# Performance work log

Measured on AMD Instinct MI355X. Metric: run time of the kernel, lower is better.

The kernel has to match this reference:

```python
import jax, jax.numpy as jnp
import numpy as np


def setup_inputs() -> dict:
    key = jax.random.key(0)
    attn = jax.random.uniform(key, (64, 1024, 1024), dtype=jnp.float32)
    return {"attn": attn}


def reference(attn) -> jnp.ndarray:
    # attn: [B, N, N]. For each sample, group strictly-upper-triangular
    # elements by diagonal offset k = j - i (k = 1..N-2; the k = N-1
    # diagonal has a single element and is excluded, matching the torch
    # loop `for i in range(len(distance_record) - 1)`).
    # For offset k: std (unbiased, ddof=1) of diag elements scaled by
    # (N-k)/5, i.e. std(x) * (N-k)/5. Then mean over k, then mean over B.
    B, N = attn.shape[0], attn.shape[1]
    ii = jnp.arange(N)
    off = ii[None, :] - ii[:, None]              # [N, N], j - i
    upper = off >= 1                              # strict upper triangle
    seg = jnp.where(upper, off, 0).reshape(-1)    # segment id per element
    m = upper.reshape(-1).astype(attn.dtype)      # mask lower/diag to 0

    x = attn.reshape(B, -1) * m                   # [B, N*N]
    segsum = lambda v: jax.ops.segment_sum(v, seg, num_segments=N)
    s1 = jax.vmap(segsum)(x)                      # [B, N] per-offset sums
    s2 = jax.vmap(segsum)(x * x)                  # [B, N] per-offset sum sq

    n = (N - jnp.arange(N)).astype(attn.dtype)    # count per offset k
    mean = s1 / n
    denom = jnp.maximum(n - 1.0, 1.0)             # ddof=1; guard k=N-1 (excluded)
    var = jnp.maximum(s2 - n * mean * mean, 0.0) / denom
    std = jnp.sqrt(var) * (n / 5.0)               # std of scaled values

    per_sample = jnp.mean(std[:, 1:N - 1], axis=1)  # offsets 1..N-2
    return jnp.mean(per_sample)
```

## Files before the change

kernel.cpp:

```cpp
#include <hip/hip_runtime.h>


#define NN 1024
#define NB 64
#define W 1032

__global__ __launch_bounds__(256) void diag_pass1(
    const float* __restrict__ attn, float* __restrict__ ws) {
  const int b  = blockIdx.x >> 3;
  const int c0 = blockIdx.x & 7;
  const int t  = threadIdx.x;
  int p = (4 - (c0 & 3)) & 3; if (p == 0) p = 4;

  const float* __restrict__ base = attn + ((size_t)b << 20);
  const size_t stride = (size_t)16 * (NN + 1);

  const int qB = 255 - t;
  float a1x=0.f,a1y=0.f,a1z=0.f,a1w=0.f,a2x=0.f,a2y=0.f,a2z=0.f,a2w=0.f;
  float b1x=0.f,b1y=0.f,b1z=0.f,b1w=0.f,b2x=0.f,b2y=0.f,b2z=0.f,b2w=0.f;

  #pragma unroll
  for (int h = 0; h < 2; ++h) {
    const int c = c0 + 8 * h;
    const float* __restrict__ rowc = base + (size_t)c * (NN + 1);

    const int dfA = 1020 - c - p - 4 * t;
    const int TfA = (dfA >= 0) ? ((dfA >> 4) + 1) : 0;
    const int SaA = (TfA + 1) >> 1;
    {
      const float* ptr = rowc + (p + 4 * t);
      #pragma unroll 8
      for (int m = 0; m < SaA; ++m) {
        const float4 v = *reinterpret_cast<const float4*>(ptr + (size_t)m * stride);
        a1x += v.x; a2x += v.x * v.x;
        a1y += v.y; a2y += v.y * v.y;
        a1z += v.z; a2z += v.z * v.z;
        a1w += v.w; a2w += v.w * v.w;
      }
    }

    const int dfB = 4 * t - c - p;
    const int TfB = (dfB >= 0) ? ((dfB >> 4) + 1) : 0;
    const int SaB = (TfB + 1) >> 1;
    {
      const float* ptr = rowc + (p + 4 * qB);
      #pragma unroll 8
      for (int m = SaB; m < TfB; ++m) {
        const float4 v = *reinterpret_cast<const float4*>(ptr + (size_t)m * stride);
        b1x += v.x; b2x += v.x * v.x;
        b1y += v.y; b2y += v.y * v.y;
        b1z += v.z; b2z += v.z * v.z;
        b1w += v.w; b2w += v.w * v.w;
      }
    }
  }

  __shared__ float4 lb1[256], lb2[256];
  lb1[qB] = make_float4(b1x, b1y, b1z, b1w);
  lb2[qB] = make_float4(b2x, b2y, b2z, b2w);
  __syncthreads();
  const float4 f1 = lb1[t];
  const float4 f2 = lb2[t];
  a1x += f1.x; a1y += f1.y; a1z += f1.z; a1w += f1.w;
  a2x += f2.x; a2y += f2.y; a2z += f2.z; a2w += f2.w;

  float* __restrict__ w1 = ws + (size_t)blockIdx.x * (2 * W);
  *reinterpret_cast<float4*>(w1 + 4 * t)     = make_float4(a1x,a1y,a1z,a1w);
  *reinterpret_cast<float4*>(w1 + W + 4 * t) = make_float4(a2x,a2y,a2z,a2w);

  const int e = t >> 6;
  if (e >= 1 && e < p) {
    const int l = t & 63;
    float e1 = 0.f, e2 = 0.f;
    #pragma unroll
    for (int h = 0; h < 2; ++h) {
      const int i = c0 + 8 * h + 16 * l;
      if (i + e < NN) {
        const float x = base[(size_t)i * (NN + 1) + e];
        e1 += x; e2 += x * x;
      }
    }
    #pragma unroll
    for (int s = 1; s < 64; s <<= 1) {
      e1 += __shfl_xor(e1, s);
      e2 += __shfl_xor(e2, s);
    }
    if (l == 0) {
      w1[1024 + e]     = e1;
      w1[W + 1024 + e] = e2;
    }
  }
}

__global__ __launch_bounds__(256) void diag_pass2(
    const float* __restrict__ ws, float* __restrict__ part) {
  const int b  = blockIdx.x >> 4;
  const int kg = blockIdx.x & 15;
  const int t  = threadIdx.x;
  const int kk = t & 63;
  const int cg = t >> 6;
  const int k  = kg * 64 + kk;

  int p = (4 - cg) & 3; if (p == 0) p = 4;
  const int idx = (k >= p) ? (k - p) : (1024 + k);

  float s1 = 0.f, s2 = 0.f;
  #pragma unroll
  for (int c = cg; c < 8; c += 4) {
    const float* __restrict__ w0 = ws + (size_t)(b * 8 + c) * (2 * W);
    s1 += w0[idx];
    s2 += w0[W + idx];
  }

  __shared__ float r1[256], r2[256];
  r1[t] = s1; r2[t] = s2;
  __syncthreads();
  if (t < 128) { r1[t] += r1[t + 128]; r2[t] += r2[t + 128]; }
  __syncthreads();
  if (t < 64) {
    s1 = r1[t] + r1[t + 64];
    s2 = r2[t] + r2[t + 64];
    float acc = 0.f;
    if (k >= 1 && k <= NN - 2) {
      const float n = (float)(NN - k);
      const float mean = s1 / n;
      const float var = fmaxf(s2 - n * mean * mean, 0.f) / (n - 1.f);
      acc = sqrtf(var) * (n * 0.2f);
    }
    #pragma unroll
    for (int s = 32; s > 0; s >>= 1) acc += __shfl_down(acc, s);
    if (t == 0) part[blockIdx.x] = acc;
  }
}

__global__ __launch_bounds__(256) void diag_pass3(
    const float* __restrict__ part, float* __restrict__ out) {
  const int t = threadIdx.x;
  float v = part[t] + part[t + 256] + part[t + 512] + part[t + 768];
  __shared__ float red[256];
  red[t] = v;
  __syncthreads();
  #pragma unroll
  for (int s = 128; s > 0; s >>= 1) {
    if (t < s) red[t] += red[t + s];
    __syncthreads();
  }
  if (t == 0) out[0] = red[0] * (1.0f / (1022.0f * 64.0f));
}

extern "C" void kernel_launch(void* const* d_in, const int* in_sizes, int n_in,
                              void* d_out, int out_size, void* d_ws, size_t ws_size,
                              hipStream_t stream) {
  const float* attn = (const float*)d_in[0];
  float* out = (float*)d_out;
  float* ws = (float*)d_ws;

  float* part = ws + (size_t)NB * 8 * 2 * W;

  diag_pass1<<<NB * 8, 256, 0, stream>>>(attn, ws);
  diag_pass2<<<NB * 16, 256, 0, stream>>>(ws, part);
  diag_pass3<<<1, 256, 0, stream>>>(part, out);
}
```

Baseline: 36.68 us.

## Rework diagonal pass to contiguous row bands with per-thread phase accumulators

Pass 1 now gives each block two contiguous 64-row bands, one from the top and one from the bottom of the matrix, which balances the triangular work. It replaces the strided diagonal walk across 16 rows. Each thread reads along rows with four alignment phases and keeps 7 partial sums, which are combined in shared memory into per-offset sums with an explicit fix-up for small offsets. This aims to improve memory locality and load balance, and it simplifies indexing in pass 2. The cost is more shared memory, extra reduction logic and branchy bounds checks per row.

```diff
diff --git a/kernel.cpp b/kernel.cpp
--- a/kernel.cpp
+++ b/kernel.cpp
@@ -3,91 +3,100 @@
 
 #define NN 1024
 #define NB 64
-#define W 1032
+#define WP 1032
 
 __global__ __launch_bounds__(256) void diag_pass1(
     const float* __restrict__ attn, float* __restrict__ ws) {
-  const int b  = blockIdx.x >> 3;
-  const int c0 = blockIdx.x & 7;
-  const int t  = threadIdx.x;
-  int p = (4 - (c0 & 3)) & 3; if (p == 0) p = 4;
+  const int b = blockIdx.x >> 3;
+  const int u = blockIdx.x & 7;
+  const int t = threadIdx.x;
+  const float* __restrict__ base = attn + ((size_t)b << 20);
 
-  const float* __restrict__ base = attn + ((size_t)b << 20);
-  const size_t stride = (size_t)16 * (NN + 1);
+  const int topi = 64 * u;
+  const int boti = 960 - 64 * u;
 
-  const int qB = 255 - t;
-  float a1x=0.f,a1y=0.f,a1z=0.f,a1w=0.f,a2x=0.f,a2y=0.f,a2z=0.f,a2w=0.f;
-  float b1x=0.f,b1y=0.f,b1z=0.f,b1w=0.f,b2x=0.f,b2y=0.f,b2z=0.f,b2w=0.f;
+  float s1[7] = {0.f,0.f,0.f,0.f,0.f,0.f,0.f};
+  float s2[7] = {0.f,0.f,0.f,0.f,0.f,0.f,0.f};
 
+#define ROW1(i, P)                                                        \
+  {                                                                       \
+    const int lim = 1024 - (i) - (P);                                     \
+    if (4 * t < lim) {                                                    \
+      const float4 v = *reinterpret_cast<const float4*>(                  \
+          base + (size_t)(i) * 1025 + (P) + 4 * t);                       \
+      s1[(P) - 1] += v.x; s2[(P) - 1] += v.x * v.x;                       \
+      s1[(P)    ] += v.y; s2[(P)    ] += v.y * v.y;                       \
+      s1[(P) + 1] += v.z; s2[(P) + 1] += v.z * v.z;                       \
+      s1[(P) + 2] += v.w; s2[(P) + 2] += v.w * v.w;                       \
+    }                                                                     \
+  }
+#define ROW4(i0)                                                          \
+  { ROW1((i0), 4) ROW1((i0) + 1, 3) ROW1((i0) + 2, 2) ROW1((i0) + 3, 1) }
+
+  #pragma unroll 2
+  for (int g = 0; g < 16; ++g) {
+    ROW4(topi + 4 * g)
+    ROW4(boti + 4 * g)
+  }
+#undef ROW4
+#undef ROW1
+
+  __shared__ float L1[7 * 256], L2[7 * 256];
+  __shared__ float Eb[8];
   #pragma unroll
-  for (int h = 0; h < 2; ++h) {
-    const int c = c0 + 8 * h;
-    const float* __restrict__ rowc = base + (size_t)c * (NN + 1);
-
-    const int dfA = 1020 - c - p - 4 * t;
-    const int TfA = (dfA >= 0) ? ((dfA >> 4) + 1) : 0;
-    const int SaA = (TfA + 1) >> 1;
-    {
-      const float* ptr = rowc + (p + 4 * t);
-      #pragma unroll 8
-      for (int m = 0; m < SaA; ++m) {
-        const float4 v = *reinterpret_cast<const float4*>(ptr + (size_t)m * stride);
-        a1x += v.x; a2x += v.x * v.x;
-        a1y += v.y; a2y += v.y * v.y;
-        a1z += v.z; a2z += v.z * v.z;
-        a1w += v.w; a2w += v.w * v.w;
-      }
-    }
-
-    const int dfB = 4 * t - c - p;
-    const int TfB = (dfB >= 0) ? ((dfB >> 4) + 1) : 0;
-    const int SaB = (TfB + 1) >> 1;
-    {
-      const float* ptr = rowc + (p + 4 * qB);
-      #pragma unroll 8
-      for (int m = SaB; m < TfB; ++m) {
-        const float4 v = *reinterpret_cast<const float4*>(ptr + (size_t)m * stride);
-        b1x += v.x; b2x += v.x * v.x;
-        b1y += v.y; b2y += v.y * v.y;
-        b1z += v.z; b2z += v.z * v.z;
-        b1w += v.w; b2w += v.w * v.w;
-      }
-    }
+  for (int bq = 0; bq < 7; ++bq) {
+    L1[bq * 256 + t] = s1[bq];
+    L2[bq * 256 + t] = s2[bq];
   }
 
-  __shared__ float4 lb1[256], lb2[256];
-  lb1[qB] = make_float4(b1x, b1y, b1z, b1w);
-  lb2[qB] = make_float4(b2x, b2y, b2z, b2w);
-  __syncthreads();
-  const float4 f1 = lb1[t];
-  const float4 f2 = lb2[t];
-  a1x += f1.x; a1y += f1.y; a1z += f1.z; a1w += f1.w;
-  a2x += f2.x; a2y += f2.y; a2z += f2.z; a2w += f2.w;
-
-  float* __restrict__ w1 = ws + (size_t)blockIdx.x * (2 * W);
-  *reinterpret_cast<float4*>(w1 + 4 * t)     = make_float4(a1x,a1y,a1z,a1w);
-  *reinterpret_cast<float4*>(w1 + W + 4 * t) = make_float4(a2x,a2y,a2z,a2w);
-
-  const int e = t >> 6;
-  if (e >= 1 && e < p) {
-    const int l = t & 63;
-    float e1 = 0.f, e2 = 0.f;
+  if (t >= 192) {
+    const int l = t - 192;
+    float E11 = 0.f, E12 = 0.f, E13 = 0.f;
+    float E21 = 0.f, E22 = 0.f, E23 = 0.f;
     #pragma unroll
-    for (int h = 0; h < 2; ++h) {
-      const int i = c0 + 8 * h + 16 * l;
-      if (i + e < NN) {
-        const float x = base[(size_t)i * (NN + 1) + e];
-        e1 += x; e2 += x * x;
-      }
+    for (int h = 0; h < 3; ++h) {
+      const int m = l + 64 * h;
+      const int grp = m / 6;
+      const int idx = m % 6;
+      const int dr = idx < 3 ? 0 : (idx < 5 ? 1 : 2);
+      const int ee = idx < 3 ? idx + 1 : (idx < 5 ? idx - 2 : 1);
+      const int i = (grp < 16 ? topi + 4 * grp : boti + 4 * (grp - 16)) + dr;
+      float x = 0.f;
+      if (i + ee < 1024) x = base[(size_t)i * 1025 + ee];
+      const float xx = x * x;
+      if (ee == 1)      { E11 += x; E21 += xx; }
+      else if (ee == 2) { E12 += x; E22 += xx; }
+      else              { E13 += x; E23 += xx; }
     }
     #pragma unroll
     for (int s = 1; s < 64; s <<= 1) {
-      e1 += __shfl_xor(e1, s);
-      e2 += __shfl_xor(e2, s);
+      E11 += __shfl_xor(E11, s); E21 += __shfl_xor(E21, s);
+      E12 += __shfl_xor(E12, s); E22 += __shfl_xor(E22, s);
+      E13 += __shfl_xor(E13, s); E23 += __shfl_xor(E23, s);
     }
     if (l == 0) {
-      w1[1024 + e]     = e1;
-      w1[W + 1024 + e] = e2;
+      Eb[1] = E11; Eb[2] = E12; Eb[3] = E13;
+      Eb[5] = E21; Eb[6] = E22; Eb[7] = E23;
+    }
+  }
+  __syncthreads();
+
+  float* __restrict__ wout = ws + (size_t)blockIdx.x * (2 * WP);
+  #pragma unroll
+  for (int j = 0; j < 4; ++j) {
+    const int k = 1 + t + 256 * j;
+    if (k <= 1023) {
+      const int b0 = (k - 1) & 3;
+      const int t0 = (k - 1) >> 2;
+      float v1 = L1[b0 * 256 + t0];
+      float v2 = L2[b0 * 256 + t0];
+      if (b0 <= 2 && t0 >= 1) {
+        v1 += L1[(b0 + 4) * 256 + t0 - 1];
+        v2 += L2[(b0 + 4) * 256 + t0 - 1];
+      }
+      if (k <= 3) { v1 += Eb[k]; v2 += Eb[4 + k]; }
+      wout[k]      = v1;
+      wout[WP + k] = v2;
     }
   }
 }
@@ -101,15 +110,12 @@
   const int cg = t >> 6;
   const int k  = kg * 64 + kk;
 
-  int p = (4 - cg) & 3; if (p == 0) p = 4;
-  const int idx = (k >= p) ? (k - p) : (1024 + k);
-
   float s1 = 0.f, s2 = 0.f;
   #pragma unroll
   for (int c = cg; c < 8; c += 4) {
-    const float* __restrict__ w0 = ws + (size_t)(b * 8 + c) * (2 * W);
-    s1 += w0[idx];
-    s2 += w0[W + idx];
+    const float* __restrict__ w0 = ws + (size_t)(b * 8 + c) * (2 * WP);
+    s1 += w0[k];
+    s2 += w0[WP + k];
   }
 
   __shared__ float r1[256], r2[256];
@@ -155,7 +161,7 @@
   float* out = (float*)d_out;
   float* ws = (float*)d_ws;
 
-  float* part = ws + (size_t)NB * 8 * 2 * W;
+  float* part = ws + (size_t)NB * 8 * 2 * WP;
 
   diag_pass1<<<NB * 8, 256, 0, stream>>>(attn, ws);
   diag_pass2<<<NB * 16, 256, 0, stream>>>(ws, part);
```

Result: slower. 61.99 us (+69.0%).
